# Kernel optimization log

Hardware: AMD Instinct MI355X
Metric: run time of the kernel (lower is better)

Reference implementation:

```python
import jax, jax.numpy as jnp
import numpy as np

D_MODEL = 768
D_STATE = 64
HEADDIM = 64
CHUNK = 64
EXPAND = 2
D_CONV = 4
D_INNER = EXPAND * D_MODEL          # 1536
NHEADS = D_INNER // HEADDIM         # 24
CONV_CH = D_INNER + 2 * D_STATE     # 1664
D_IN_PROJ = 2 * D_INNER + 2 * D_STATE + NHEADS  # 3224
EPS = 1e-5


def segsum(x):
    # x: (..., T) -> (..., T, T); entry [i, j] = sum_{k=j+1..i} x[k] for i>=j, -inf above diag
    T = x.shape[-1]
    cs = jnp.cumsum(x, axis=-1)
    seg = cs[..., :, None] - cs[..., None, :]
    mask = jnp.tril(jnp.ones((T, T), dtype=bool))
    return jnp.where(mask, seg, -jnp.inf)


def ssd(x, A, B, C, chunk):
    # x: (b, L, h, p), A: (b, L, h), B/C: (b, L, n)
    b, L, h, p = x.shape
    nc = L // chunk
    x = x.reshape(b, nc, chunk, h, p)
    A = A.reshape(b, nc, chunk, h).transpose(0, 3, 1, 2)   # (b, h, nc, l)
    B = B.reshape(b, nc, chunk, -1)
    C = C.reshape(b, nc, chunk, -1)
    A_cs = jnp.cumsum(A, axis=-1)                          # (b, h, nc, l)
    Lm = jnp.exp(segsum(A))                                # (b, h, nc, l, s)
    # intra-chunk (diagonal) term
    Y_diag = jnp.einsum('bcln,bcsn,bhcls,bcshp->bclhp', C, B, Lm, x)
    # per-chunk states
    decay_states = jnp.exp(A_cs[..., -1:] - A_cs)          # (b, h, nc, l)
    states = jnp.einsum('bcln,bhcl,bclhp->bchpn', B, decay_states, x)
    states = jnp.concatenate([jnp.zeros_like(states[:, :1]), states], axis=1)
    # inter-chunk recurrence via segsum over chunk totals
    chunk_sums = jnp.pad(A_cs[..., -1], ((0, 0), (0, 0), (1, 0)))
    decay_chunk = jnp.exp(segsum(chunk_sums))              # (b, h, nc+1, nc+1)
    new_states = jnp.einsum('bhzc,bchpn->bzhpn', decay_chunk, states)
    states = new_states[:, :-1]                            # (b, nc, h, p, n)
    Y_off = jnp.einsum('bcln,bchpn,bhcl->bclhp', C, states, jnp.exp(A_cs))
    return (Y_diag + Y_off).reshape(b, L, h, p)


def setup_inputs() -> dict:
    key = jax.random.key(0)
    ks = jax.random.split(key, 6)
    b, L = 2, 4096
    u = jax.random.normal(ks[0], (b, L, D_MODEL), dtype=jnp.float32)
    W_in = jax.random.normal(ks[1], (D_IN_PROJ, D_MODEL), dtype=jnp.float32) * (D_MODEL ** -0.5)
    conv_w = jax.random.normal(ks[2], (CONV_CH, 1, D_CONV), dtype=jnp.float32) * 0.3
    conv_b = jnp.zeros((CONV_CH,), dtype=jnp.float32)
    dt_bias = jnp.zeros((NHEADS,), dtype=jnp.float32)
    A_log = jax.random.normal(ks[3], (NHEADS,), dtype=jnp.float32) * 0.1
    D = jnp.ones((NHEADS,), dtype=jnp.float32)
    norm_w = jnp.ones((D_INNER,), dtype=jnp.float32)
    W_out = jax.random.normal(ks[4], (D_MODEL, D_INNER), dtype=jnp.float32) * (D_INNER ** -0.5)
    return {'u': u, 'W_in': W_in, 'conv_w': conv_w, 'conv_b': conv_b,
            'dt_bias': dt_bias, 'A_log': A_log, 'D': D, 'norm_w': norm_w, 'W_out': W_out}


def reference(u, W_in, conv_w, conv_b, dt_bias, A_log, D, norm_w, W_out):
    b, L, _ = u.shape
    zxbcdt = u @ W_in.T                                    # (b, L, d_in_proj)
    z = zxbcdt[..., :D_INNER]
    xBC = zxbcdt[..., D_INNER:D_INNER + CONV_CH]
    dt = jax.nn.softplus(zxbcdt[..., -NHEADS:] + dt_bias)  # (b, L, h)
    # causal depthwise conv (left pad d_conv-1, matches torch pad+slice)
    xBC = jax.lax.conv_general_dilated(
        xBC.transpose(0, 2, 1), conv_w, (1,), [(D_CONV - 1, 0)],
        dimension_numbers=('NCH', 'OIH', 'NCH'), feature_group_count=CONV_CH)
    xBC = jax.nn.silu(xBC.transpose(0, 2, 1) + conv_b)
    x = xBC[..., :D_INNER].reshape(b, L, NHEADS, HEADDIM)
    Bm = xBC[..., D_INNER:D_INNER + D_STATE]
    Cm = xBC[..., -D_STATE:]
    A = -jnp.exp(A_log)                                    # (h,)
    y = ssd(x * dt[..., None], A * dt, Bm, Cm, CHUNK)
    y = y + x * D[None, None, :, None]
    y = y.reshape(b, L, D_INNER)
    # gated RMSNorm
    y = y * jax.nn.silu(z)
    y = y * jax.lax.rsqrt(jnp.mean(y * y, axis=-1, keepdims=True) + EPS) * norm_w
    return y @ W_out.T
```

## Files before the change

### kernel.cpp

```cpp
#include <hip/hip_runtime.h>

typedef __attribute__((ext_vector_type(4))) float f4;
typedef __attribute__((ext_vector_type(8))) short bfx8;
typedef __attribute__((ext_vector_type(4))) float f32x4;
typedef __attribute__((ext_vector_type(4))) unsigned int u32x4;
typedef __attribute__((ext_vector_type(4))) unsigned short u16x4;
typedef __attribute__((ext_vector_type(8))) unsigned short u16x8;
typedef unsigned short ushort_t;

#define DM 768
#define DINNER 1536
#define NH 24
#define XBCW 1664
#define DINPROJ 3224
#define NPAD1 3328
#define NCHUNK 64
#define BROWS 8192
#define PADB 72

__device__ inline ushort_t f2bf(float f) {
    unsigned u = __builtin_bit_cast(unsigned, f);
    unsigned r = (u + 0x7FFF + ((u >> 16) & 1)) >> 16;
    return (ushort_t)r;
}
__device__ inline float bf2f(ushort_t u) {
    return __builtin_bit_cast(float, (unsigned)u << 16);
}
__device__ inline void gl16(const void* g, void* l) {
    __builtin_amdgcn_global_load_lds((const __attribute__((address_space(1))) void*)g,
                                     (__attribute__((address_space(3))) void*)l, 16, 0, 0);
}

__global__ __launch_bounds__(256) void fill_kernel(float* out, int n, float v) {
    int i = blockIdx.x * 256 + threadIdx.x;
    if (i < n) out[i] = v;
}

__global__ __launch_bounds__(256) void cvt_kernel(const float* __restrict__ in,
                                                  ushort_t* __restrict__ outp, long n4) {
    long i = (long)blockIdx.x * 256 + threadIdx.x;
    if (i >= n4) return;
    f4 v = *(const f4*)&in[i * 4];
    u16x4 o;
    o[0] = f2bf(v[0]); o[1] = f2bf(v[1]); o[2] = f2bf(v[2]); o[3] = f2bf(v[3]);
    *(u16x4*)&outp[i * 4] = o;
}

__global__ __launch_bounds__(256) void cvt_pad_kernel(const float* __restrict__ in,
                                                      ushort_t* __restrict__ outp) {
    long q = (long)blockIdx.x * 256 + threadIdx.x;
    if (q >= (long)NPAD1 * 192) return;
    int row = (int)(q / 192);
    int cq = (int)(q % 192);
    u16x4 o = {0, 0, 0, 0};
    if (row < DINPROJ) {
        f4 v = *(const f4*)&in[(long)row * DM + cq * 4];
        o[0] = f2bf(v[0]); o[1] = f2bf(v[1]); o[2] = f2bf(v[2]); o[3] = f2bf(v[3]);
    }
    *(u16x4*)&outp[q * 4] = o;
}

template <int EPI>
__global__ __launch_bounds__(256) void gemm_bt(const ushort_t* __restrict__ A,
                                               const ushort_t* __restrict__ B,
                                               float* __restrict__ C,
                                               int K, int ldc,
                                               ushort_t* __restrict__ zbf,
                                               ushort_t* __restrict__ xbcbf,
                                               float* __restrict__ dtbT,
                                               const float* __restrict__ dt_bias) {
    __shared__ __align__(16) ushort_t As[3][128 * 32];
    __shared__ __align__(16) ushort_t Bs[3][128 * 32];
    int tid = threadIdx.x;
    int lane = tid & 63;
    int w = tid >> 6;
    int wr = w >> 1, wc = w & 1;
    int m0 = blockIdx.y * 128;
    int n0 = blockIdx.x * 128;
    int r16 = lane & 15, kg = lane >> 4;

    int row0 = tid >> 2, cof0 = (tid & 3) * 8;
    const ushort_t* a0 = &A[(long)(m0 + row0) * K + cof0];
    const ushort_t* a1 = &A[(long)(m0 + row0 + 64) * K + cof0];
    const ushort_t* b0 = &B[(long)(n0 + row0) * K + cof0];
    const ushort_t* b1 = &B[(long)(n0 + row0 + 64) * K + cof0];
    char* asb[3] = {(char*)&As[0][0] + w * 1024, (char*)&As[1][0] + w * 1024,
                    (char*)&As[2][0] + w * 1024};
    char* bsb[3] = {(char*)&Bs[0][0] + w * 1024, (char*)&Bs[1][0] + w * 1024,
                    (char*)&Bs[2][0] + w * 1024};

    f32x4 acc[4][4] = {};
    int nk = K >> 5;

    auto issue = [&](int t) {
        int k = t << 5;
        int bi = t % 3;
        gl16(a0 + k, asb[bi]); gl16(a1 + k, asb[bi] + 4096);
        gl16(b0 + k, bsb[bi]); gl16(b1 + k, bsb[bi] + 4096);
    };
    issue(0);
    issue(1);

    for (int t = 0; t < nk; ++t) {
        if (t + 1 < nk) {
            asm volatile("s_waitcnt vmcnt(4)" ::: "memory");
        } else {
            asm volatile("s_waitcnt vmcnt(0)" ::: "memory");
        }
        __builtin_amdgcn_s_barrier();
        __builtin_amdgcn_sched_barrier(0);
        if (t + 2 < nk) issue(t + 2);
        const ushort_t* Asc = &As[t % 3][0];
        const ushort_t* Bsc = &Bs[t % 3][0];
        bfx8 af[4], bfr[4];
#pragma unroll
        for (int i = 0; i < 4; ++i) {
            af[i] = *(const bfx8*)&Asc[(wr * 64 + i * 16 + r16) * 32 + kg * 8];
            bfr[i] = *(const bfx8*)&Bsc[(wc * 64 + i * 16 + r16) * 32 + kg * 8];
        }
#pragma unroll
        for (int i = 0; i < 4; ++i)
#pragma unroll
            for (int j = 0; j < 4; ++j)
                acc[i][j] = __builtin_amdgcn_mfma_f32_16x16x32_bf16(af[i], bfr[j], acc[i][j], 0, 0, 0);
    }

#pragma unroll
    for (int i = 0; i < 4; ++i) {
        int rowb = m0 + wr * 64 + i * 16 + kg * 4;
#pragma unroll
        for (int j = 0; j < 4; ++j) {
            int col = n0 + wc * 64 + j * 16 + r16;
            if (EPI == 0) {
#pragma unroll
                for (int q = 0; q < 4; ++q)
                    C[(long)(rowb + q) * ldc + col] = acc[i][j][q];
            } else {
                if (n0 < DINNER) {
#pragma unroll
                    for (int q = 0; q < 4; ++q)
                        zbf[(long)(rowb + q) * DINNER + col] = f2bf(acc[i][j][q]);
                } else if (n0 < 3200) {
#pragma unroll
                    for (int q = 0; q < 4; ++q)
                        xbcbf[(long)(rowb + q) * XBCW + col - DINNER] = f2bf(acc[i][j][q]);
                } else if (col < DINPROJ) {
                    int h = col - 3200;
                    float bias = dt_bias[h];
#pragma unroll
                    for (int q = 0; q < 4; ++q) {
                        float v = acc[i][j][q] + bias;
                        float d = (v > 20.f) ? v : log1pf(__expf(v));
                        dtbT[(long)h * BROWS + rowb + q] = d;
                    }
                }
            }
        }
    }
}

__global__ __launch_bounds__(256) void conv_kernel(const ushort_t* __restrict__ xin,
                                                   const float* __restrict__ cw,
                                                   const float* __restrict__ cb,
                                                   ushort_t* __restrict__ xbc) {
    int ch = blockIdx.y * 256 + threadIdx.x;
    int row = blockIdx.x;
    if (ch >= XBCW) return;
    int b = row >> 12;
    int l = row & 4095;
    float acc = cb[ch];
#pragma unroll
    for (int k = 0; k < 4; ++k) {
        int ll = l - 3 + k;
        if (ll >= 0)
            acc += cw[ch * 4 + k] * bf2f(xin[(long)(b * 4096 + ll) * XBCW + ch]);
    }
    float s = acc / (1.f + __expf(-acc));
    xbc[(long)row * XBCW + ch] = f2bf(s);
}

__global__ __launch_bounds__(256) void acs_kernel(const float* __restrict__ dtbT,
                                                  const float* __restrict__ A_log,
                                                  float* __restrict__ acs,
                                                  float* __restrict__ Tsum) {
    int bh = blockIdx.x;
    int b = bh / NH, h = bh % NH;
    int t = threadIdx.x;
    int lane = t & 63;
    float A = -__expf(A_log[h]);
    const float* dp = &dtbT[(long)h * BROWS + b * 4096];
#pragma unroll
    for (int it = 0; it < 16; ++it) {
        int c = (t >> 6) + 4 * it;
        float v = A * dp[c * 64 + lane];
#pragma unroll
        for (int off = 1; off < 64; off <<= 1) {
            float u = __shfl_up(v, off, 64);
            if (lane >= off) v += u;
        }
        acs[((long)bh * NCHUNK + c) * 64 + lane] = v;
        if (lane == 63) Tsum[bh * NCHUNK + c] = v;
    }
}

__global__ __launch_bounds__(256) void states_kernel(const ushort_t* __restrict__ xbc,
                                                     const float* __restrict__ dtbT,
                                                     const float* __restrict__ acs,
                                                     const float* __restrict__ Tsum,
                                                     ushort_t* __restrict__ states) {
    int h = blockIdx.x, c = blockIdx.y, b = blockIdx.z;
    __shared__ __align__(16) ushort_t Wt[64 * PADB];
    __shared__ __align__(16) ushort_t Bt[64 * PADB];
    int t = threadIdx.x;
    long rowg0 = (long)b * 4096 + c * 64;
    long acsb = ((long)(b * NH + h) * NCHUNK + c) * 64;
    float T = Tsum[(b * NH + h) * NCHUNK + c];
#pragma unroll
    for (int i = 0; i < 2; ++i) {
        int q = t + 256 * i;
        int l = q >> 3, sg = q & 7;
        const ushort_t* rp = &xbc[(rowg0 + l) * (long)XBCW];
        float dec = dtbT[(long)h * BROWS + rowg0 + l] * __expf(T - acs[acsb + l]);
        u16x8 xv = *(const u16x8*)&rp[h * 64 + sg * 8];
        u16x8 bv = *(const u16x8*)&rp[DINNER + sg * 8];
#pragma unroll
        for (int jj = 0; jj < 8; ++jj) {
            Wt[(sg * 8 + jj) * PADB + l] = f2bf(bf2f(xv[jj]) * dec);
            Bt[(sg * 8 + jj) * PADB + l] = bv[jj];
        }
    }
    __syncthreads();
    int w = t >> 6, lane = t & 63;
    int r16 = lane & 15, kg = lane >> 4;
    bfx8 aw[2];
#pragma unroll
    for (int kk = 0; kk < 2; ++kk)
        aw[kk] = *(const bfx8*)&Wt[(w * 16 + r16) * PADB + kk * 32 + kg * 8];
    f32x4 acc[4] = {};
#pragma unroll
    for (int j = 0; j < 4; ++j)
#pragma unroll
        for (int kk = 0; kk < 2; ++kk) {
            bfx8 bb = *(const bfx8*)&Bt[(j * 16 + r16) * PADB + kk * 32 + kg * 8];
            acc[j] = __builtin_amdgcn_mfma_f32_16x16x32_bf16(aw[kk], bb, acc[j], 0, 0, 0);
        }
    __syncthreads();
#pragma unroll
    for (int j = 0; j < 4; ++j)
#pragma unroll
        for (int q = 0; q < 4; ++q)
            Wt[(w * 16 + kg * 4 + q) * PADB + j * 16 + r16] = f2bf(acc[j][q]);
    __syncthreads();
    long ob = ((long)(b * NH + h) * NCHUNK + c) * 4096;
#pragma unroll
    for (int i = 0; i < 2; ++i) {
        int q = t + 256 * i;
        int p = q >> 3, sg = q & 7;
        *(u16x8*)&states[ob + p * 64 + sg * 8] = *(const u16x8*)&Wt[p * PADB + sg * 8];
    }
}

__global__ __launch_bounds__(256) void scan_kernel(const float* __restrict__ Tsum,
                                                   ushort_t* __restrict__ states) {
    int e = blockIdx.x * 256 + threadIdx.x;
    int h = blockIdx.y, b = blockIdx.z;
    long base = ((long)(b * NH + h)) * NCHUNK * 4096 + e;
    const float* Tp = &Tsum[(b * NH + h) * NCHUNK];
    float acc = 0.f;
    for (int c = 0; c < NCHUNK; ++c) {
        float cur = bf2f(states[base + (long)c * 4096]);
        states[base + (long)c * 4096] = f2bf(acc);
        acc = __expf(Tp[c]) * acc + cur;
    }
}

__global__ __launch_bounds__(256) void yfull_kernel(const ushort_t* __restrict__ xbc,
                                                    const float* __restrict__ dtbT,
                                                    const float* __restrict__ acs,
                                                    const ushort_t* __restrict__ sprev,
                                                    ushort_t* __restrict__ ybuf) {
    int h = blockIdx.x, c = blockIdx.y, b = blockIdx.z;
    __shared__ __align__(16) ushort_t Cb[64 * PADB];
    __shared__ __align__(16) ushort_t Bb[64 * PADB];
    __shared__ __align__(16) ushort_t Xt[64 * PADB];
    __shared__ __align__(16) ushort_t Sp[64 * PADB];
    __shared__ __align__(16) ushort_t Sm[64 * PADB];
    __shared__ float sAcs[64], sE[64];
    int t = threadIdx.x;
    long rowg0 = (long)b * 4096 + c * 64;
    long acsb = ((long)(b * NH + h) * NCHUNK + c) * 64;
    long spb = ((long)(b * NH + h) * NCHUNK + c) * 4096;
    if (t < 64) {
        float a = acs[acsb + t];
        sAcs[t] = a;
        sE[t] = __expf(a);
    }
#pragma unroll
    for (int i = 0; i < 2; ++i) {
        int q = t + 256 * i;
        int l = q >> 3, sg = q & 7;
        const ushort_t* rp = &xbc[(rowg0 + l) * (long)XBCW];
        *(u16x8*)&Cb[l * PADB + sg * 8] = *(const u16x8*)&rp[1600 + sg * 8];
        *(u16x8*)&Bb[l * PADB + sg * 8] = *(const u16x8*)&rp[DINNER + sg * 8];
        float dtv = dtbT[(long)h * BROWS + rowg0 + l];
        u16x8 xv = *(const u16x8*)&rp[h * 64 + sg * 8];
#pragma unroll
        for (int jj = 0; jj < 8; ++jj)
            Xt[(sg * 8 + jj) * PADB + l] = f2bf(bf2f(xv[jj]) * dtv);
        *(u16x8*)&Sp[l * PADB + sg * 8] = *(const u16x8*)&sprev[spb + l * 64 + sg * 8];
    }
    __syncthreads();
    int w = t >> 6, lane = t & 63;
    int r16 = lane & 15, kg = lane >> 4;
    bfx8 ac[2];
#pragma unroll
    for (int kk = 0; kk < 2; ++kk)
        ac[kk] = *(const bfx8*)&Cb[(w * 16 + r16) * PADB + kk * 32 + kg * 8];
    f32x4 s_acc[4] = {};
#pragma unroll
    for (int j = 0; j < 4; ++j)
#pragma unroll
        for (int kk = 0; kk < 2; ++kk) {
            bfx8 bb = *(const bfx8*)&Bb[(j * 16 + r16) * PADB + kk * 32 + kg * 8];
            s_acc[j] = __builtin_amdgcn_mfma_f32_16x16x32_bf16(ac[kk], bb, s_acc[j], 0, 0, 0);
        }
#pragma unroll
    for (int j = 0; j < 4; ++j)
#pragma unroll
        for (int q = 0; q < 4; ++q) {
            int l = w * 16 + kg * 4 + q;
            int s = j * 16 + r16;
            float v = s_acc[j][q];
            v = (s <= l) ? v * __expf(sAcs[l] - sAcs[s]) : 0.f;
            Sm[l * PADB + s] = f2bf(v);
        }
    __syncthreads();
    bfx8 as[2];
#pragma unroll
    for (int kk = 0; kk < 2; ++kk)
        as[kk] = *(const bfx8*)&Sm[(w * 16 + r16) * PADB + kk * 32 + kg * 8];
    f32x4 d_acc[4] = {}, o_acc[4] = {};
#pragma unroll
    for (int j = 0; j < 4; ++j)
#pragma unroll
        for (int kk = 0; kk < 2; ++kk) {
            bfx8 xb = *(const bfx8*)&Xt[(j * 16 + r16) * PADB + kk * 32 + kg * 8];
            d_acc[j] = __builtin_amdgcn_mfma_f32_16x16x32_bf16(as[kk], xb, d_acc[j], 0, 0, 0);
            bfx8 sb = *(const bfx8*)&Sp[(j * 16 + r16) * PADB + kk * 32 + kg * 8];
            o_acc[j] = __builtin_amdgcn_mfma_f32_16x16x32_bf16(ac[kk], sb, o_acc[j], 0, 0, 0);
        }
#pragma unroll
    for (int j = 0; j < 4; ++j)
#pragma unroll
        for (int q = 0; q < 4; ++q) {
            int l = w * 16 + kg * 4 + q;
            int p = j * 16 + r16;
            Bb[l * PADB + p] = f2bf(d_acc[j][q] + sE[l] * o_acc[j][q]);
        }
    __syncthreads();
#pragma unroll
    for (int i = 0; i < 2; ++i) {
        int q = t + 256 * i;
        int l = q >> 3, sg = q & 7;
        *(u16x8*)&ybuf[(rowg0 + l) * (long)DINNER + h * 64 + sg * 8] =
            *(const u16x8*)&Bb[l * PADB + sg * 8];
    }
}

__global__ __launch_bounds__(256) void norm_kernel(const ushort_t* __restrict__ ybuf,
                                                   const ushort_t* __restrict__ xbc,
                                                   const ushort_t* __restrict__ zbf,
                                                   const float* __restrict__ Dp,
                                                   const float* __restrict__ normw,
                                                   ushort_t* __restrict__ ybf) {
    int row = blockIdx.x;
    int t = threadIdx.x;
    float g[6];
    float ss = 0.f;
#pragma unroll
    for (int i = 0; i < 6; ++i) {
        int j = t + 256 * i;
        int h = j >> 6;
        float x = bf2f(xbc[(long)row * XBCW + j]);
        float yy = bf2f(ybuf[(long)row * DINNER + j]) + x * Dp[h];
        float z = bf2f(zbf[(long)row * DINNER + j]);
        float gz = z / (1.f + __expf(-z));
        float v = yy * gz;
        g[i] = v;
        ss += v * v;
    }
#pragma unroll
    for (int o = 32; o > 0; o >>= 1) ss += __shfl_xor(ss, o, 64);
    __shared__ float wsum[4];
    __shared__ float sscale;
    int w = t >> 6;
    if ((t & 63) == 0) wsum[w] = ss;
    __syncthreads();
    if (t == 0) {
        float tot = wsum[0] + wsum[1] + wsum[2] + wsum[3];
        sscale = rsqrtf(tot / (float)DINNER + 1e-5f);
    }
    __syncthreads();
    float sc = sscale;
#pragma unroll
    for (int i = 0; i < 6; ++i) {
        int j = t + 256 * i;
        ybf[(long)row * DINNER + j] = f2bf(g[i] * sc * normw[j]);
    }
}

extern "C" void kernel_launch(void* const* d_in, const int* in_sizes, int n_in,
                              void* d_out, int out_size, void* d_ws, size_t ws_size,
                              hipStream_t stream) {
    const float* u = (const float*)d_in[0];
    const float* W_in = (const float*)d_in[1];
    const float* conv_w = (const float*)d_in[2];
    const float* conv_b = (const float*)d_in[3];
    const float* dt_bias = (const float*)d_in[4];
    const float* A_log = (const float*)d_in[5];
    const float* Dp = (const float*)d_in[6];
    const float* norm_w = (const float*)d_in[7];
    const float* W_out = (const float*)d_in[8];
    float* out = (float*)d_out;

    char* ws = (char*)d_ws;
    size_t off = 0;
    auto alloc = [&](size_t bytes) {
        void* p = ws + off;
        off += (bytes + 255) & ~(size_t)255;
        return p;
    };
    ushort_t* zbf = (ushort_t*)alloc((size_t)BROWS * DINNER * 2);
    ushort_t* xbcrawbf = (ushort_t*)alloc((size_t)BROWS * XBCW * 2);
    ushort_t* xbc = (ushort_t*)alloc((size_t)BROWS * XBCW * 2);
    float* dtbT = (float*)alloc((size_t)NH * BROWS * 4);
    float* acs = (float*)alloc((size_t)2 * NH * NCHUNK * 64 * 4);
    float* Tsum = (float*)alloc((size_t)2 * NH * NCHUNK * 4);
    ushort_t* states = (ushort_t*)alloc((size_t)2 * NH * NCHUNK * 4096 * 2);
    ushort_t* ybuf = (ushort_t*)alloc((size_t)BROWS * DINNER * 2);
    ushort_t* ybf = xbcrawbf;
    ushort_t* ubf = ybuf;
    ushort_t* winbf = states;
    ushort_t* woutbf = states;

    if (off > ws_size) {
        fill_kernel<<<(out_size + 255) / 256, 256, 0, stream>>>(out, out_size, 12345.0f);
        return;
    }

    cvt_kernel<<<(BROWS * DM / 4 + 255) / 256, 256, 0, stream>>>(u, ubf, (long)BROWS * DM / 4);
    cvt_pad_kernel<<<((long)NPAD1 * 192 + 255) / 256, 256, 0, stream>>>(W_in, winbf);

    gemm_bt<1><<<dim3(26, 64), 256, 0, stream>>>(ubf, winbf, nullptr, DM, 0,
                                                 zbf, xbcrawbf, dtbT, dt_bias);

    conv_kernel<<<dim3(BROWS, 7), 256, 0, stream>>>(xbcrawbf, conv_w, conv_b, xbc);

    acs_kernel<<<2 * NH, 256, 0, stream>>>(dtbT, A_log, acs, Tsum);
    states_kernel<<<dim3(NH, NCHUNK, 2), 256, 0, stream>>>(xbc, dtbT, acs, Tsum, states);
    scan_kernel<<<dim3(16, NH, 2), 256, 0, stream>>>(Tsum, states);
    yfull_kernel<<<dim3(NH, NCHUNK, 2), 256, 0, stream>>>(xbc, dtbT, acs, states, ybuf);

    norm_kernel<<<BROWS, 256, 0, stream>>>(ybuf, xbc, zbf, Dp, norm_w, ybf);

    cvt_kernel<<<(DM * DINNER / 4 + 255) / 256, 256, 0, stream>>>(W_out, woutbf, (long)DM * DINNER / 4);
    gemm_bt<0><<<dim3(6, 64), 256, 0, stream>>>(ybf, woutbf, out, DINNER, DM,
                                                nullptr, nullptr, nullptr, nullptr);
}
```

Before: 278.7 us.

## Add transposed xBC buffer for SSD kernels and remap GEMM block order

Adds a transpose kernel that writes x and B channels of the conv output in channel-major order. The states and yfull kernels then fill their transposed LDS tiles with vectorized 16-byte loads and stores instead of scalar strided LDS writes, and the per-row decay and dt factors are hoisted into shared memory. The GEMM also remaps block IDs in groups of 8, presumably to spread adjacent tiles across XCDs for cache locality. The cost is an extra kernel launch plus a write and reread of roughly 26 MB of transposed data.

```diff
diff --git a/kernel.cpp b/kernel.cpp
--- a/kernel.cpp
+++ b/kernel.cpp
@@ -75,8 +75,13 @@
     int lane = tid & 63;
     int w = tid >> 6;
     int wr = w >> 1, wc = w & 1;
-    int m0 = blockIdx.y * 128;
-    int n0 = blockIdx.x * 128;
+    int gx = gridDim.x;
+    int nwg = gx * gridDim.y;
+    int id = blockIdx.y * gx + blockIdx.x;
+    int per = nwg >> 3;
+    int id2 = (id & 7) * per + (id >> 3);
+    int m0 = (id2 / gx) * 128;
+    int n0 = (id2 % gx) * 128;
     int r16 = lane & 15, kg = lane >> 4;
 
     int row0 = tid >> 2, cof0 = (tid & 3) * 8;
@@ -179,6 +184,31 @@
     xbc[(long)row * XBCW + ch] = f2bf(s);
 }
 
+__global__ __launch_bounds__(256) void xt_kernel(const ushort_t* __restrict__ xbc,
+                                                 ushort_t* __restrict__ xT) {
+    __shared__ ushort_t tile[64][PADB];
+    int rt = blockIdx.x;
+    int ct = blockIdx.y;
+    int t = threadIdx.x;
+#pragma unroll
+    for (int i = 0; i < 2; ++i) {
+        int q = t + 256 * i;
+        int r = q >> 3, cc = q & 7;
+        *(u16x8*)&tile[r][cc * 8] =
+            *(const u16x8*)&xbc[(long)(rt * 64 + r) * XBCW + ct * 64 + cc * 8];
+    }
+    __syncthreads();
+#pragma unroll
+    for (int i = 0; i < 2; ++i) {
+        int q = t + 256 * i;
+        int ch = q >> 3, sg = q & 7;
+        u16x8 o;
+#pragma unroll
+        for (int k = 0; k < 8; ++k) o[k] = tile[sg * 8 + k][ch];
+        *(u16x8*)&xT[(long)(ct * 64 + ch) * BROWS + rt * 64 + sg * 8] = o;
+    }
+}
+
 __global__ __launch_bounds__(256) void acs_kernel(const float* __restrict__ dtbT,
                                                   const float* __restrict__ A_log,
                                                   float* __restrict__ acs,
@@ -203,7 +233,7 @@
     }
 }
 
-__global__ __launch_bounds__(256) void states_kernel(const ushort_t* __restrict__ xbc,
+__global__ __launch_bounds__(256) void states_kernel(const ushort_t* __restrict__ xT,
                                                      const float* __restrict__ dtbT,
                                                      const float* __restrict__ acs,
                                                      const float* __restrict__ Tsum,
@@ -211,23 +241,25 @@
     int h = blockIdx.x, c = blockIdx.y, b = blockIdx.z;
     __shared__ __align__(16) ushort_t Wt[64 * PADB];
     __shared__ __align__(16) ushort_t Bt[64 * PADB];
+    __shared__ float sDec[64];
     int t = threadIdx.x;
     long rowg0 = (long)b * 4096 + c * 64;
     long acsb = ((long)(b * NH + h) * NCHUNK + c) * 64;
     float T = Tsum[(b * NH + h) * NCHUNK + c];
+    if (t < 64)
+        sDec[t] = dtbT[(long)h * BROWS + rowg0 + t] * __expf(T - acs[acsb + t]);
+    __syncthreads();
 #pragma unroll
     for (int i = 0; i < 2; ++i) {
         int q = t + 256 * i;
-        int l = q >> 3, sg = q & 7;
-        const ushort_t* rp = &xbc[(rowg0 + l) * (long)XBCW];
-        float dec = dtbT[(long)h * BROWS + rowg0 + l] * __expf(T - acs[acsb + l]);
-        u16x8 xv = *(const u16x8*)&rp[h * 64 + sg * 8];
-        u16x8 bv = *(const u16x8*)&rp[DINNER + sg * 8];
-#pragma unroll
-        for (int jj = 0; jj < 8; ++jj) {
-            Wt[(sg * 8 + jj) * PADB + l] = f2bf(bf2f(xv[jj]) * dec);
-            Bt[(sg * 8 + jj) * PADB + l] = bv[jj];
-        }
+        int p = q >> 3, sg = q & 7;
+        u16x8 xv = *(const u16x8*)&xT[(long)(h * 64 + p) * BROWS + rowg0 + sg * 8];
+        u16x8 wv;
+#pragma unroll
+        for (int j = 0; j < 8; ++j) wv[j] = f2bf(bf2f(xv[j]) * sDec[sg * 8 + j]);
+        *(u16x8*)&Wt[p * PADB + sg * 8] = wv;
+        *(u16x8*)&Bt[p * PADB + sg * 8] =
+            *(const u16x8*)&xT[(long)(DINNER + p) * BROWS + rowg0 + sg * 8];
     }
     __syncthreads();
     int w = t >> 6, lane = t & 63;
@@ -275,6 +307,7 @@
 }
 
 __global__ __launch_bounds__(256) void yfull_kernel(const ushort_t* __restrict__ xbc,
+                                                    const ushort_t* __restrict__ xT,
                                                     const float* __restrict__ dtbT,
                                                     const float* __restrict__ acs,
                                                     const ushort_t* __restrict__ sprev,
@@ -285,7 +318,7 @@
     __shared__ __align__(16) ushort_t Xt[64 * PADB];
     __shared__ __align__(16) ushort_t Sp[64 * PADB];
     __shared__ __align__(16) ushort_t Sm[64 * PADB];
-    __shared__ float sAcs[64], sE[64];
+    __shared__ float sAcs[64], sE[64], sDt[64];
     int t = threadIdx.x;
     long rowg0 = (long)b * 4096 + c * 64;
     long acsb = ((long)(b * NH + h) * NCHUNK + c) * 64;
@@ -294,7 +327,9 @@
         float a = acs[acsb + t];
         sAcs[t] = a;
         sE[t] = __expf(a);
-    }
+        sDt[t] = dtbT[(long)h * BROWS + rowg0 + t];
+    }
+    __syncthreads();
 #pragma unroll
     for (int i = 0; i < 2; ++i) {
         int q = t + 256 * i;
@@ -302,11 +337,11 @@
         const ushort_t* rp = &xbc[(rowg0 + l) * (long)XBCW];
         *(u16x8*)&Cb[l * PADB + sg * 8] = *(const u16x8*)&rp[1600 + sg * 8];
         *(u16x8*)&Bb[l * PADB + sg * 8] = *(const u16x8*)&rp[DINNER + sg * 8];
-        float dtv = dtbT[(long)h * BROWS + rowg0 + l];
-        u16x8 xv = *(const u16x8*)&rp[h * 64 + sg * 8];
-#pragma unroll
-        for (int jj = 0; jj < 8; ++jj)
-            Xt[(sg * 8 + jj) * PADB + l] = f2bf(bf2f(xv[jj]) * dtv);
+        u16x8 xv = *(const u16x8*)&xT[(long)(h * 64 + l) * BROWS + rowg0 + sg * 8];
+        u16x8 xo;
+#pragma unroll
+        for (int j = 0; j < 8; ++j) xo[j] = f2bf(bf2f(xv[j]) * sDt[sg * 8 + j]);
+        *(u16x8*)&Xt[l * PADB + sg * 8] = xo;
         *(u16x8*)&Sp[l * PADB + sg * 8] = *(const u16x8*)&sprev[spb + l * 64 + sg * 8];
     }
     __syncthreads();
@@ -433,6 +468,7 @@
     ushort_t* zbf = (ushort_t*)alloc((size_t)BROWS * DINNER * 2);
     ushort_t* xbcrawbf = (ushort_t*)alloc((size_t)BROWS * XBCW * 2);
     ushort_t* xbc = (ushort_t*)alloc((size_t)BROWS * XBCW * 2);
+    ushort_t* xT = (ushort_t*)alloc((size_t)1600 * BROWS * 2);
     float* dtbT = (float*)alloc((size_t)NH * BROWS * 4);
     float* acs = (float*)alloc((size_t)2 * NH * NCHUNK * 64 * 4);
     float* Tsum = (float*)alloc((size_t)2 * NH * NCHUNK * 4);
@@ -455,11 +491,12 @@
                                                  zbf, xbcrawbf, dtbT, dt_bias);
 
     conv_kernel<<<dim3(BROWS, 7), 256, 0, stream>>>(xbcrawbf, conv_w, conv_b, xbc);
+    xt_kernel<<<dim3(128, 25), 256, 0, stream>>>(xbc, xT);
 
     acs_kernel<<<2 * NH, 256, 0, stream>>>(dtbT, A_log, acs, Tsum);
-    states_kernel<<<dim3(NH, NCHUNK, 2), 256, 0, stream>>>(xbc, dtbT, acs, Tsum, states);
+    states_kernel<<<dim3(NH, NCHUNK, 2), 256, 0, stream>>>(xT, dtbT, acs, Tsum, states);
     scan_kernel<<<dim3(16, NH, 2), 256, 0, stream>>>(Tsum, states);
-    yfull_kernel<<<dim3(NH, NCHUNK, 2), 256, 0, stream>>>(xbc, dtbT, acs, states, ybuf);
+    yfull_kernel<<<dim3(NH, NCHUNK, 2), 256, 0, stream>>>(xbc, xT, dtbT, acs, states, ybuf);
 
     norm_kernel<<<BROWS, 256, 0, stream>>>(ybuf, xbc, zbf, Dp, norm_w, ybf);
 
```

After: 280.3 us. About the same (+0.6%).
